# Kernel optimization log

Measured on AMD Instinct MI355X. Metric: run time of the kernel, lower is better.

Reference implementation:

```python
import jax, jax.numpy as jnp
import numpy as np

TEMP = 0.1
THRESH = 0.9
HARD_RATIO = 0.5
B = 8192
K = max(1, int(B * HARD_RATIO))  # 4096 hard negatives per row


def _normalize(x):
    return x / jnp.linalg.norm(x, axis=-1, keepdims=True)


def _projector(x, W1, b1, W2, b2):
    # Linear -> ReLU -> Linear
    h = jax.nn.relu(x @ W1 + b1)
    return h @ W2 + b2


def _hard_negative_mining(sim):
    bsz = sim.shape[0]
    eye = jnp.eye(bsz, dtype=bool)
    neg_sim = jnp.where(eye, -jnp.inf, sim)
    noise = (neg_sim > THRESH / TEMP) & ~eye
    ranking = jnp.where(noise, -jnp.inf, neg_sim)
    _, idx = jax.lax.top_k(ranking, K)  # (B, K) hard negative indices
    hard = jnp.zeros((bsz, bsz), dtype=bool).at[jnp.arange(bsz)[:, None], idx].set(True)
    # noise weight (0.5) overrides hard weight (1.5), as in torch sequential assignment
    w = jnp.where(noise, 0.5, jnp.where(hard, 1.5, 1.0)).astype(sim.dtype)
    return sim * w


def _modal_loss(id_emb, feat, Wa, ba, W1, b1, W2, b2, mw):
    modal_feat = feat @ Wa + ba                       # adapter
    modal_proj = _normalize(_projector(modal_feat, W1, b1, W2, b2))
    id_proj = _normalize(_projector(id_emb, W1, b1, W2, b2))
    sim = (id_proj @ modal_proj.T) / TEMP             # (B, B)
    sim = _hard_negative_mining(sim)
    ce = -jnp.diagonal(jax.nn.log_softmax(sim, axis=-1))  # labels = arange
    return jnp.mean(ce * mw)


def setup_inputs() -> dict:
    key = jax.random.key(0)
    ks = jax.random.split(key, 20)
    HID, PROJ = 1024, 512

    def lin(k, i, o):
        return (jax.random.normal(k, (i, o), jnp.float32) / np.sqrt(i)).astype(jnp.float32)

    return {
        'id_embeddings': jax.random.normal(ks[0], (B, HID), jnp.float32),
        'text_feat': jax.random.normal(ks[1], (B, 768), jnp.float32),
        'visual_feat': jax.random.normal(ks[2], (B, 2048), jnp.float32),
        'modal_weights': jax.random.uniform(ks[3], (B, 2), jnp.float32),
        'Wa_t': lin(ks[4], 768, HID),  'ba_t': jnp.zeros((HID,), jnp.float32),
        'Wa_v': lin(ks[5], 2048, HID), 'ba_v': jnp.zeros((HID,), jnp.float32),
        'W1_t': lin(ks[6], HID, HID),  'b1_t': jnp.zeros((HID,), jnp.float32),
        'W2_t': lin(ks[7], HID, PROJ), 'b2_t': jnp.zeros((PROJ,), jnp.float32),
        'W1_v': lin(ks[8], HID, HID),  'b1_v': jnp.zeros((HID,), jnp.float32),
        'W2_v': lin(ks[9], HID, PROJ), 'b2_v': jnp.zeros((PROJ,), jnp.float32),
    }


def reference(id_embeddings, text_feat, visual_feat, modal_weights,
              Wa_t, ba_t, Wa_v, ba_v,
              W1_t, b1_t, W2_t, b2_t,
              W1_v, b1_v, W2_v, b2_v):
    # sorted(modal_features.keys()) -> ['text', 'visual'] (idx 0, 1)
    l_text = _modal_loss(id_embeddings, text_feat, Wa_t, ba_t, W1_t, b1_t, W2_t, b2_t, modal_weights[:, 0])
    l_vis = _modal_loss(id_embeddings, visual_feat, Wa_v, ba_v, W1_v, b1_v, W2_v, b2_v, modal_weights[:, 1])
    return (l_text + l_vis) / 2.0
```

## Files before the change

kernel.cpp:

```cpp
#include <hip/hip_runtime.h>
#include <math.h>
#include <stdint.h>


typedef __attribute__((ext_vector_type(4))) float  floatx4;
typedef __attribute__((ext_vector_type(8))) __bf16 bf16x8;

__device__ __forceinline__ unsigned short f2bf(float f)
{
    unsigned u = __float_as_uint(f);
    unsigned r = (u + 0x7FFFu + ((u >> 16) & 1u)) >> 16;
    return (unsigned short)r;
}

__device__ __forceinline__ float bf2f(unsigned short u)
{
    return __uint_as_float((unsigned)u << 16);
}

__device__ __forceinline__ void gld_lds16(const void* g, void* l)
{
    __builtin_amdgcn_global_load_lds(
        (const __attribute__((address_space(1))) void*)g,
        (__attribute__((address_space(3))) void*)(uint32_t)(uintptr_t)l,
        16, 0, 0);
}

#define EPW  136
#define EPW2 264


__device__ __forceinline__ void stage_half256(
    const unsigned short* __restrict__ g, int ld, int k0,
    unsigned short* lds, int t)
{
#pragma unroll
    for (int it = 0; it < 2; ++it) {
        const int li  = it * 512 + t;
        const int row = li >> 3;
        const int c   = (li & 7) ^ (row & 7);
        gld_lds16(g + (size_t)row * ld + k0 + c * 8, lds + li * 8);
    }
}

__global__ __launch_bounds__(512, 2) void gemm_bt_256(
    const unsigned short* __restrict__ A, int lda,
    const unsigned short* __restrict__ B, int ldb,
    unsigned short* __restrict__ C, int ldc, int M, int N, int K,
    const float* __restrict__ bias, int relu, float scale)
{
    __shared__ __align__(16) unsigned short smem[65536];

    const int num_n = N >> 8;
    const int per   = gridDim.x >> 3;
    const int pid   = blockIdx.x;
    const int npid  = (pid & 7) * per + (pid >> 3);
    const int width = 4 * num_n;
    const int group = npid / width;
    const int rem   = npid - group * width;
    const int pm    = group * 4 + (rem & 3);
    const int pn    = rem >> 2;

    const int t    = threadIdx.x;
    const int lane = t & 63;
    const int w    = t >> 6;
    const int wr   = w >> 2;
    const int wc   = w & 3;
    const size_t m0 = (size_t)pm * 256;
    const size_t n0 = (size_t)pn * 256;

    floatx4 acc[8][4] = {};

    const unsigned short* Abase = A + m0 * (size_t)lda;
    const unsigned short* Bbase = B + n0 * (size_t)ldb;

    int aoff[8][2], boff[4][2];
#pragma unroll
    for (int ks = 0; ks < 2; ++ks) {
        const int cc = ks * 4 + (lane >> 4);
#pragma unroll
        for (int i = 0; i < 8; ++i) {
            const int rr = i * 16 + (lane & 15);
            aoff[i][ks] = wr * 8192 + rr * 64 + ((cc ^ (rr & 7)) << 3);
        }
#pragma unroll
        for (int j = 0; j < 4; ++j) {
            const int rb = wc * 64 + j * 16 + (lane & 15);
            const int rr = rb & 127;
            boff[j][ks] = 16384 + (rb >> 7) * 8192 + rr * 64
                        + ((cc ^ (rr & 7)) << 3);
        }
    }

    const int NT = K >> 6;

    stage_half256(Abase, lda, 0, smem, t);
    stage_half256(Abase + (size_t)128 * lda, lda, 0, smem + 8192, t);
    stage_half256(Bbase, ldb, 0, smem + 16384, t);
    stage_half256(Bbase + (size_t)128 * ldb, ldb, 0, smem + 24576, t);

    for (int kt = 0; kt < NT; ++kt) {
        unsigned short* cb = smem + (kt & 1) * 32768;
        unsigned short* nb = smem + ((kt + 1) & 1) * 32768;
        const int kn = (kt + 1) << 6;

        if (kt + 1 < NT) {
            stage_half256(Abase, lda, kn, nb, t);
            stage_half256(Abase + (size_t)128 * lda, lda, kn, nb + 8192, t);
            asm volatile("s_waitcnt vmcnt(4)" ::: "memory");
        } else {
            asm volatile("s_waitcnt vmcnt(0)" ::: "memory");
        }
        __builtin_amdgcn_sched_barrier(0);
        __builtin_amdgcn_s_barrier();
        __builtin_amdgcn_sched_barrier(0);

        {
            bf16x8 af[8], bf[4];
#pragma unroll
            for (int i = 0; i < 8; ++i) af[i] = *(const bf16x8*)(cb + aoff[i][0]);
#pragma unroll
            for (int j = 0; j < 4; ++j) bf[j] = *(const bf16x8*)(cb + boff[j][0]);
            __builtin_amdgcn_s_setprio(1);
#pragma unroll
            for (int i = 0; i < 8; ++i)
#pragma unroll
                for (int j = 0; j < 4; ++j)
                    acc[i][j] = __builtin_amdgcn_mfma_f32_16x16x32_bf16(
                        af[i], bf[j], acc[i][j], 0, 0, 0);
            __builtin_amdgcn_s_setprio(0);
        }
        __builtin_amdgcn_sched_barrier(0);
        __builtin_amdgcn_s_barrier();
        __builtin_amdgcn_sched_barrier(0);

        if (kt + 1 < NT) {
            stage_half256(Bbase, ldb, kn, nb + 16384, t);
            stage_half256(Bbase + (size_t)128 * ldb, ldb, kn, nb + 24576, t);
        }
        {
            bf16x8 af[8], bf[4];
#pragma unroll
            for (int i = 0; i < 8; ++i) af[i] = *(const bf16x8*)(cb + aoff[i][1]);
#pragma unroll
            for (int j = 0; j < 4; ++j) bf[j] = *(const bf16x8*)(cb + boff[j][1]);
            __builtin_amdgcn_s_setprio(1);
#pragma unroll
            for (int i = 0; i < 8; ++i)
#pragma unroll
                for (int j = 0; j < 4; ++j)
                    acc[i][j] = __builtin_amdgcn_mfma_f32_16x16x32_bf16(
                        af[i], bf[j], acc[i][j], 0, 0, 0);
            __builtin_amdgcn_s_setprio(0);
        }
        __builtin_amdgcn_sched_barrier(0);
        __builtin_amdgcn_s_barrier();
        __builtin_amdgcn_sched_barrier(0);
    }

    const int col   = lane & 15;
    const int rquad = (lane >> 4) * 4;
#pragma unroll
    for (int h = 0; h < 2; ++h) {
        if (wr == h) {
#pragma unroll
            for (int j = 0; j < 4; ++j) {
                const int lc = wc * 64 + j * 16 + col;
                const float bv = bias ? bias[n0 + lc] : 0.0f;
#pragma unroll
                for (int i = 0; i < 8; ++i) {
                    const int lr0 = i * 16 + rquad;
#pragma unroll
                    for (int r = 0; r < 4; ++r) {
                        float v = acc[i][j][r] * scale + bv;
                        if (relu) v = fmaxf(v, 0.0f);
                        smem[(lr0 + r) * EPW2 + lc] = f2bf(v);
                    }
                }
            }
        }
        __syncthreads();
        const int cr = t >> 2;
        const int cq = t & 3;
#pragma unroll
        for (int q = 0; q < 8; ++q) {
            const int chunk = cq + q * 4;
            uint4 v = *(const uint4*)(smem + cr * EPW2 + chunk * 8);
            *(uint4*)(C + (m0 + h * 128 + cr) * (size_t)ldc + n0 + chunk * 8) = v;
        }
        __syncthreads();
    }
}


__device__ __forceinline__ void stage_tile(
    const unsigned short* __restrict__ g, int ld, int k0,
    unsigned short* lds, int t)
{
#pragma unroll
    for (int it = 0; it < 4; ++it) {
        const int row = it * 32 + (t >> 3);
        const int c   = (t & 7) ^ ((t >> 3) & 7);
        gld_lds16(g + (size_t)row * ld + k0 + c * 8,
                  lds + (it * 256 + t) * 8);
    }
}

__global__ __launch_bounds__(256) void gemm_bt_mfma(
    const unsigned short* __restrict__ A, int lda,
    const unsigned short* __restrict__ B, int ldb,
    unsigned short* __restrict__ C, int ldc, int M, int N, int K,
    const float* __restrict__ bias, int relu, float scale)
{
    __shared__ __align__(16) unsigned short smem[32768];

    const int num_n = N >> 7;
    const int per   = gridDim.x >> 3;
    const int pid   = blockIdx.x;
    const int npid  = (pid & 7) * per + (pid >> 3);
    const int width = 4 * num_n;
    const int group = npid / width;
    const int rem   = npid - group * width;
    const int pm    = group * 4 + (rem & 3);
    const int pn    = rem >> 2;

    const int t    = threadIdx.x;
    const int lane = t & 63;
    const int w    = t >> 6;
    const int wr   = w >> 1;
    const int wc   = w & 1;
    const size_t m0 = (size_t)pm * 128;
    const size_t n0 = (size_t)pn * 128;

    floatx4 acc[4][4] = {};

    const unsigned short* Abase = A + m0 * (size_t)lda;
    const unsigned short* Bbase = B + n0 * (size_t)ldb;

    int aoff[4][2], boff[4][2];
#pragma unroll
    for (int i = 0; i < 4; ++i) {
        const int ra = wr * 64 + i * 16 + (lane & 15);
        const int rb = wc * 64 + i * 16 + (lane & 15);
#pragma unroll
        for (int ks = 0; ks < 2; ++ks) {
            const int cc = ks * 4 + (lane >> 4);
            aoff[i][ks] = ra * 64 + ((cc ^ (ra & 7)) << 3);
            boff[i][ks] = rb * 64 + ((cc ^ (rb & 7)) << 3);
        }
    }

    const int NT = K >> 6;

    stage_tile(Abase, lda, 0, smem, t);
    stage_tile(Bbase, ldb, 0, smem + 8192, t);

    int cur = 0;
    for (int kt = 0; kt < NT; ++kt) {
        if (kt + 1 < NT) {
            unsigned short* nb = smem + (cur ^ 1) * 16384;
            stage_tile(Abase, lda, (kt + 1) << 6, nb, t);
            stage_tile(Bbase, ldb, (kt + 1) << 6, nb + 8192, t);
            asm volatile("s_waitcnt vmcnt(8)" ::: "memory");
        } else {
            asm volatile("s_waitcnt vmcnt(0)" ::: "memory");
        }
        __builtin_amdgcn_sched_barrier(0);
        __builtin_amdgcn_s_barrier();
        __builtin_amdgcn_sched_barrier(0);

        const unsigned short* As = smem + cur * 16384;
        const unsigned short* Bs = As + 8192;

        bf16x8 af[4][2], bfr[4][2];
#pragma unroll
        for (int i = 0; i < 4; ++i) {
#pragma unroll
            for (int ks = 0; ks < 2; ++ks) {
                af[i][ks]  = *(const bf16x8*)(As + aoff[i][ks]);
                bfr[i][ks] = *(const bf16x8*)(Bs + boff[i][ks]);
            }
        }
#pragma unroll
        for (int i = 0; i < 4; ++i)
#pragma unroll
            for (int j = 0; j < 4; ++j)
#pragma unroll
                for (int ks = 0; ks < 2; ++ks)
                    acc[i][j] = __builtin_amdgcn_mfma_f32_16x16x32_bf16(
                        af[i][ks], bfr[j][ks], acc[i][j], 0, 0, 0);

        asm volatile("s_waitcnt lgkmcnt(0)" ::: "memory");
        __builtin_amdgcn_sched_barrier(0);
        __builtin_amdgcn_s_barrier();
        __builtin_amdgcn_sched_barrier(0);
        cur ^= 1;
    }

    const int col   = lane & 15;
    const int rquad = (lane >> 4) * 4;
#pragma unroll
    for (int j = 0; j < 4; ++j) {
        const int lc = wc * 64 + j * 16 + col;
        const float bv = bias ? bias[n0 + lc] : 0.0f;
#pragma unroll
        for (int i = 0; i < 4; ++i) {
            const int lr0 = wr * 64 + i * 16 + rquad;
#pragma unroll
            for (int r = 0; r < 4; ++r) {
                float v = acc[i][j][r] * scale + bv;
                if (relu) v = fmaxf(v, 0.0f);
                smem[(lr0 + r) * EPW + lc] = f2bf(v);
            }
        }
    }
    __syncthreads();
#pragma unroll
    for (int h = 0; h < 2; ++h) {
        const int cr = h * 64 + (t >> 2);
        const int cq = t & 3;
#pragma unroll
        for (int q = 0; q < 4; ++q) {
            const int chunk = cq + q * 4;
            uint4 v = *(const uint4*)(smem + cr * EPW + chunk * 8);
            *(uint4*)(C + (m0 + cr) * (size_t)ldc + n0 + chunk * 8) = v;
        }
    }
}

__global__ __launch_bounds__(256) void cast_bf16_kernel(
    const float* __restrict__ in, unsigned short* __restrict__ out, int n4)
{
    const int i = blockIdx.x * 256 + threadIdx.x;
    if (i < n4) {
        float4 v = *(const float4*)(in + (size_t)i * 4);
        ushort4 o;
        o.x = f2bf(v.x); o.y = f2bf(v.y); o.z = f2bf(v.z); o.w = f2bf(v.w);
        *(ushort4*)(out + (size_t)i * 4) = o;
    }
}

__global__ __launch_bounds__(256) void transpose_cast_kernel(
    const float* __restrict__ W, unsigned short* __restrict__ WT, int K, int N)
{
    __shared__ float tile[32][33];
    const int k0 = blockIdx.y * 32;
    const int n0 = blockIdx.x * 32;
    const int tr = threadIdx.x >> 3;
    const int tc = (threadIdx.x & 7) * 4;

    float4 v = *(const float4*)(W + (size_t)(k0 + tr) * N + n0 + tc);
    tile[tr][tc + 0] = v.x;
    tile[tr][tc + 1] = v.y;
    tile[tr][tc + 2] = v.z;
    tile[tr][tc + 3] = v.w;
    __syncthreads();

    ushort4 o;
    o.x = f2bf(tile[tc + 0][tr]);
    o.y = f2bf(tile[tc + 1][tr]);
    o.z = f2bf(tile[tc + 2][tr]);
    o.w = f2bf(tile[tc + 3][tr]);
    *(ushort4*)(WT + (size_t)(n0 + tr) * K + k0 + tc) = o;
}

__global__ __launch_bounds__(128) void normalize_bf16_kernel(
    unsigned short* __restrict__ X)
{
    const int r = blockIdx.x;
    const int t = threadIdx.x;
    unsigned short* row = X + (size_t)r * 512;
    ushort4 u = *(const ushort4*)(row + t * 4);
    float x0 = bf2f(u.x), x1 = bf2f(u.y), x2 = bf2f(u.z), x3 = bf2f(u.w);
    float ss = x0 * x0 + x1 * x1 + x2 * x2 + x3 * x3;
#pragma unroll
    for (int off = 32; off > 0; off >>= 1) ss += __shfl_down(ss, off, 64);
    __shared__ float sred[2];
    if ((t & 63) == 0) sred[t >> 6] = ss;
    __syncthreads();
    float inv = 1.0f / sqrtf(sred[0] + sred[1]);
    ushort4 o;
    o.x = f2bf(x0 * inv); o.y = f2bf(x1 * inv);
    o.z = f2bf(x2 * inv); o.w = f2bf(x3 * inv);
    *(ushort4*)(row + t * 4) = o;
}

__global__ __launch_bounds__(256, 4) void row_loss_kernel(
    const unsigned short* __restrict__ S, int row_base,
    const float* __restrict__ mw, int midx, float* __restrict__ accum)
{
    __shared__ unsigned hist[4096];
    __shared__ unsigned wtot[4];
    __shared__ float fred[4];
    __shared__ unsigned sh_b;
    __shared__ float sh_diag;

    const int t    = threadIdx.x;
    const int lane = t & 63;
    const int wv   = t >> 6;
    const int i    = row_base + blockIdx.x;
    const unsigned short* Srow = S + (size_t)blockIdx.x * 8192;

    for (int b = t; b < 4096; b += 256) hist[b] = 0;

    uint4 raw[4];
#pragma unroll
    for (int seg = 0; seg < 4; ++seg)
        raw[seg] = *(const uint4*)(Srow + seg * 2048 + t * 8);
    __syncthreads();

#pragma unroll
    for (int seg = 0; seg < 4; ++seg) {
        const unsigned short* e = (const unsigned short*)&raw[seg];
#pragma unroll
        for (int q = 0; q < 8; ++q) {
            const int j = seg * 2048 + t * 8 + q;
            const float s = bf2f(e[q]);
            if (j != i && s <= 9.0f) {
                int k = (int)((s + 10.25f) * 200.0f);
                k = k < 1 ? 1 : (k > 4095 ? 4095 : k);
                atomicAdd(&hist[k], 1u);
            }
        }
    }
    __syncthreads();

    unsigned local = 0;
#pragma unroll
    for (int q = 0; q < 16; ++q) local += hist[t * 16 + q];
    unsigned suf = local;
#pragma unroll
    for (int off = 1; off < 64; off <<= 1) {
        unsigned v = __shfl_down(suf, off, 64);
        if (lane + off < 64) suf += v;
    }
    if (lane == 0) wtot[wv] = suf;
    __syncthreads();
    unsigned wsuf = 0;
#pragma unroll
    for (int q = 0; q < 4; ++q) wsuf += (q > wv) ? wtot[q] : 0u;
    suf += wsuf;

    const unsigned target = 4096;
    const unsigned above  = suf - local;
    if (suf >= target && above < target) {
        unsigned cum = above;
        int bsel = t * 16;
#pragma unroll
        for (int q = 15; q >= 0; --q) {
            unsigned c = hist[t * 16 + q];
            if (cum + c >= target) { bsel = t * 16 + q; break; }
            cum += c;
        }
        sh_b = (unsigned)bsel;
    }
    if (t == 0 && suf < target) sh_b = 1u;
    __syncthreads();
    const unsigned bsel = sh_b;

    float lsum = 0.0f;
#pragma unroll
    for (int seg = 0; seg < 4; ++seg) {
        const unsigned short* e = (const unsigned short*)&raw[seg];
#pragma unroll
        for (int q = 0; q < 8; ++q) {
            const int j = seg * 2048 + t * 8 + q;
            const float s = bf2f(e[q]);
            bool diag  = (j == i);
            bool noise = (!diag && s > 9.0f);
            int k = (int)((s + 10.25f) * 200.0f);
            k = k < 1 ? 1 : (k > 4095 ? 4095 : k);
            bool hard = !diag && !noise && ((unsigned)k >= bsel);
            float wgt = noise ? 0.5f : (hard ? 1.5f : 1.0f);
            float ws = s * wgt;
            if (diag) sh_diag = ws;
            lsum += __expf(ws - 16.0f);
        }
    }
#pragma unroll
    for (int off = 32; off > 0; off >>= 1)
        lsum += __shfl_down(lsum, off, 64);
    if (lane == 0) fred[wv] = lsum;
    __syncthreads();
    if (t == 0) {
        float total = fred[0] + fred[1] + fred[2] + fred[3];
        float lse = 16.0f + logf(total);
        float ce = lse - sh_diag;
        atomicAdd(&accum[midx * 64 + (blockIdx.x & 63)],
                  ce * mw[(size_t)i * 2 + midx]);
    }
}

__global__ void zero_kernel(float* __restrict__ accum)
{
    if (threadIdx.x < 128) accum[threadIdx.x] = 0.0f;
}

__global__ void finalize_kernel(const float* __restrict__ accum,
                                float* __restrict__ out)
{
    float s = 0.0f;
    for (int q = 0; q < 128; ++q) s += accum[q];
    out[0] = s * (1.0f / 16384.0f);
}

extern "C" void kernel_launch(void* const* d_in, const int* in_sizes, int n_in,
                              void* d_out, int out_size, void* d_ws, size_t ws_size,
                              hipStream_t stream)
{
    (void)in_sizes; (void)n_in; (void)out_size; (void)ws_size;

    const float* id_emb = (const float*)d_in[0];
    const float* feats[2] = { (const float*)d_in[1], (const float*)d_in[2] };
    const float* mw     = (const float*)d_in[3];
    const float* Wa[2]  = { (const float*)d_in[4],  (const float*)d_in[6]  };
    const float* ba[2]  = { (const float*)d_in[5],  (const float*)d_in[7]  };
    const float* W1[2]  = { (const float*)d_in[8],  (const float*)d_in[12] };
    const float* b1[2]  = { (const float*)d_in[9],  (const float*)d_in[13] };
    const float* W2[2]  = { (const float*)d_in[10], (const float*)d_in[14] };
    const float* b2[2]  = { (const float*)d_in[11], (const float*)d_in[15] };
    const int    Fdim[2] = { 768, 2048 };

    char* p = (char*)d_ws;
    unsigned short* WaT   = (unsigned short*)p; p += (size_t)1024 * 2048 * 2;
    unsigned short* W1T   = (unsigned short*)p; p += (size_t)1024 * 1024 * 2;
    unsigned short* W2T   = (unsigned short*)p; p += (size_t)512  * 1024 * 2;
    unsigned short* X     = (unsigned short*)p; p += (size_t)16384 * 1024 * 2;
    unsigned short* featb = (unsigned short*)p; p += (size_t)8192 * 2048 * 2;
    unsigned short* H     = (unsigned short*)p; p += (size_t)16384 * 1024 * 2;
    unsigned short* PB    = (unsigned short*)p; p += (size_t)16384 * 512  * 2;
    float*          accum = (float*)p;
    unsigned short* S     = featb;

    zero_kernel<<<1, 128, 0, stream>>>(accum);

    cast_bf16_kernel<<<(8192 * 1024 / 4 + 255) / 256, 256, 0, stream>>>(
        id_emb, X + (size_t)8192 * 1024, 8192 * 1024 / 4);

    for (int m = 0; m < 2; ++m) {
        const int F = Fdim[m];

        cast_bf16_kernel<<<(8192 * F / 4 + 255) / 256, 256, 0, stream>>>(
            feats[m], featb, 8192 * F / 4);
        transpose_cast_kernel<<<dim3(1024 / 32, F / 32), 256, 0, stream>>>(
            Wa[m], WaT, F, 1024);
        transpose_cast_kernel<<<dim3(1024 / 32, 1024 / 32), 256, 0, stream>>>(
            W1[m], W1T, 1024, 1024);
        transpose_cast_kernel<<<dim3(512 / 32, 1024 / 32), 256, 0, stream>>>(
            W2[m], W2T, 1024, 512);

        gemm_bt_mfma<<<(8192 / 128) * (1024 / 128), 256, 0, stream>>>(
            featb, F, WaT, F, X, 1024, 8192, 1024, F, ba[m], 0, 1.0f);

        gemm_bt_256<<<(16384 / 256) * (1024 / 256), 512, 0, stream>>>(
            X, 1024, W1T, 1024, H, 1024, 16384, 1024, 1024, b1[m], 1, 1.0f);
        gemm_bt_mfma<<<(16384 / 128) * (512 / 128), 256, 0, stream>>>(
            H, 1024, W2T, 1024, PB, 512, 16384, 512, 1024, b2[m], 0, 1.0f);
        normalize_bf16_kernel<<<16384, 128, 0, stream>>>(PB);

        const unsigned short* mproj = PB;
        const unsigned short* iproj = PB + (size_t)8192 * 512;

        for (int c = 0; c < 2; ++c) {
            gemm_bt_256<<<(4096 / 256) * (8192 / 256), 512, 0, stream>>>(
                iproj + (size_t)c * 4096 * 512, 512, mproj, 512,
                S, 8192, 4096, 8192, 512, nullptr, 0, 10.0f);
            row_loss_kernel<<<4096, 256, 0, stream>>>(
                S, c * 4096, mw, m, accum);
        }
    }

    finalize_kernel<<<1, 1, 0, stream>>>(accum, (float*)d_out);
}
```

Before: 688.5 us.

## Split 256-tile GEMM k-loop into four phases with finer barrier staging

Restructures the main loop of the 256x256 bf16 GEMM into four compute phases of 16 MFMAs each, loading only half of the A fragments per phase. The B-tile prefetch is spread across phases. Register pressure drops from 12 live fragments to 8, and the schedule resembles ping-pong style interleaving of LDS reads, global prefetch and MFMA. The cost is more workgroup barriers per k-step, which can add synchronisation stalls.

```diff
diff --git a/kernel.cpp b/kernel.cpp
--- a/kernel.cpp
+++ b/kernel.cpp
@@ -28,6 +28,10 @@
 
 #define EPW  136
 #define EPW2 264
+
+#define SBAR() do { __builtin_amdgcn_sched_barrier(0); \
+                    __builtin_amdgcn_s_barrier();      \
+                    __builtin_amdgcn_sched_barrier(0); } while (0)
 
 
 __device__ __forceinline__ void stage_half256(
@@ -103,59 +107,75 @@
         unsigned short* cb = smem + (kt & 1) * 32768;
         unsigned short* nb = smem + ((kt + 1) & 1) * 32768;
         const int kn = (kt + 1) << 6;
-
-        if (kt + 1 < NT) {
+        const bool pf = (kt + 1) < NT;
+
+        bf16x8 af4[4], bfc[4];
+
+        if (pf) {
             stage_half256(Abase, lda, kn, nb, t);
             stage_half256(Abase + (size_t)128 * lda, lda, kn, nb + 8192, t);
             asm volatile("s_waitcnt vmcnt(4)" ::: "memory");
         } else {
             asm volatile("s_waitcnt vmcnt(0)" ::: "memory");
         }
-        __builtin_amdgcn_sched_barrier(0);
-        __builtin_amdgcn_s_barrier();
-        __builtin_amdgcn_sched_barrier(0);
-
-        {
-            bf16x8 af[8], bf[4];
-#pragma unroll
-            for (int i = 0; i < 8; ++i) af[i] = *(const bf16x8*)(cb + aoff[i][0]);
-#pragma unroll
-            for (int j = 0; j < 4; ++j) bf[j] = *(const bf16x8*)(cb + boff[j][0]);
-            __builtin_amdgcn_s_setprio(1);
-#pragma unroll
-            for (int i = 0; i < 8; ++i)
-#pragma unroll
-                for (int j = 0; j < 4; ++j)
-                    acc[i][j] = __builtin_amdgcn_mfma_f32_16x16x32_bf16(
-                        af[i], bf[j], acc[i][j], 0, 0, 0);
-            __builtin_amdgcn_s_setprio(0);
-        }
-        __builtin_amdgcn_sched_barrier(0);
-        __builtin_amdgcn_s_barrier();
-        __builtin_amdgcn_sched_barrier(0);
-
-        if (kt + 1 < NT) {
-            stage_half256(Bbase, ldb, kn, nb + 16384, t);
-            stage_half256(Bbase + (size_t)128 * ldb, ldb, kn, nb + 24576, t);
-        }
-        {
-            bf16x8 af[8], bf[4];
-#pragma unroll
-            for (int i = 0; i < 8; ++i) af[i] = *(const bf16x8*)(cb + aoff[i][1]);
-#pragma unroll
-            for (int j = 0; j < 4; ++j) bf[j] = *(const bf16x8*)(cb + boff[j][1]);
-            __builtin_amdgcn_s_setprio(1);
-#pragma unroll
-            for (int i = 0; i < 8; ++i)
-#pragma unroll
-                for (int j = 0; j < 4; ++j)
-                    acc[i][j] = __builtin_amdgcn_mfma_f32_16x16x32_bf16(
-                        af[i], bf[j], acc[i][j], 0, 0, 0);
-            __builtin_amdgcn_s_setprio(0);
-        }
-        __builtin_amdgcn_sched_barrier(0);
-        __builtin_amdgcn_s_barrier();
-        __builtin_amdgcn_sched_barrier(0);
+        SBAR();
+#pragma unroll
+        for (int i = 0; i < 4; ++i) af4[i] = *(const bf16x8*)(cb + aoff[i][0]);
+#pragma unroll
+        for (int j = 0; j < 4; ++j) bfc[j] = *(const bf16x8*)(cb + boff[j][0]);
+        SBAR();
+        __builtin_amdgcn_s_setprio(1);
+#pragma unroll
+        for (int i = 0; i < 4; ++i)
+#pragma unroll
+            for (int j = 0; j < 4; ++j)
+                acc[i][j] = __builtin_amdgcn_mfma_f32_16x16x32_bf16(
+                    af4[i], bfc[j], acc[i][j], 0, 0, 0);
+        __builtin_amdgcn_s_setprio(0);
+        SBAR();
+
+#pragma unroll
+        for (int i = 0; i < 4; ++i) af4[i] = *(const bf16x8*)(cb + aoff[4 + i][0]);
+        if (pf) stage_half256(Bbase, ldb, kn, nb + 16384, t);
+        SBAR();
+        __builtin_amdgcn_s_setprio(1);
+#pragma unroll
+        for (int i = 0; i < 4; ++i)
+#pragma unroll
+            for (int j = 0; j < 4; ++j)
+                acc[4 + i][j] = __builtin_amdgcn_mfma_f32_16x16x32_bf16(
+                    af4[i], bfc[j], acc[4 + i][j], 0, 0, 0);
+        __builtin_amdgcn_s_setprio(0);
+        SBAR();
+
+#pragma unroll
+        for (int i = 0; i < 4; ++i) af4[i] = *(const bf16x8*)(cb + aoff[i][1]);
+#pragma unroll
+        for (int j = 0; j < 4; ++j) bfc[j] = *(const bf16x8*)(cb + boff[j][1]);
+        if (pf) stage_half256(Bbase + (size_t)128 * ldb, ldb, kn, nb + 24576, t);
+        SBAR();
+        __builtin_amdgcn_s_setprio(1);
+#pragma unroll
+        for (int i = 0; i < 4; ++i)
+#pragma unroll
+            for (int j = 0; j < 4; ++j)
+                acc[i][j] = __builtin_amdgcn_mfma_f32_16x16x32_bf16(
+                    af4[i], bfc[j], acc[i][j], 0, 0, 0);
+        __builtin_amdgcn_s_setprio(0);
+        SBAR();
+
+#pragma unroll
+        for (int i = 0; i < 4; ++i) af4[i] = *(const bf16x8*)(cb + aoff[4 + i][1]);
+        SBAR();
+        __builtin_amdgcn_s_setprio(1);
+#pragma unroll
+        for (int i = 0; i < 4; ++i)
+#pragma unroll
+            for (int j = 0; j < 4; ++j)
+                acc[4 + i][j] = __builtin_amdgcn_mfma_f32_16x16x32_bf16(
+                    af4[i], bfc[j], acc[4 + i][j], 0, 0, 0);
+        __builtin_amdgcn_s_setprio(0);
+        SBAR();
     }
 
     const int col   = lane & 15;
@@ -265,9 +285,7 @@
         } else {
             asm volatile("s_waitcnt vmcnt(0)" ::: "memory");
         }
-        __builtin_amdgcn_sched_barrier(0);
-        __builtin_amdgcn_s_barrier();
-        __builtin_amdgcn_sched_barrier(0);
+        SBAR();
 
         const unsigned short* As = smem + cur * 16384;
         const unsigned short* Bs = As + 8192;
@@ -291,9 +309,7 @@
                         af[i][ks], bfr[j][ks], acc[i][j], 0, 0, 0);
 
         asm volatile("s_waitcnt lgkmcnt(0)" ::: "memory");
-        __builtin_amdgcn_sched_barrier(0);
-        __builtin_amdgcn_s_barrier();
-        __builtin_amdgcn_sched_barrier(0);
+        SBAR();
         cur ^= 1;
     }
 
```

New measurement: 717.7 us. 4.2% more time.
